# Kernel optimization log

Hardware: AMD Instinct MI355X
Metric: run time of the kernel (lower is better)

Reference implementation:

```python
import jax, jax.numpy as jnp
import numpy as np

B = 16384
FEAT_SIZES = [1000000, 1000000, 500000, 500000, 100000, 100000, 10000, 10000]
EMB_DIM = 50          # min(50, feat_size//2) for all chosen sizes
CONT_IN = 64
D = 8 * EMB_DIM + 64  # 464 = total_embedding_size + 64
H1, H2 = 256, 128     # expert/cross hidden sizes
E, T = 4, 3           # num_experts, num_tasks


def setup_inputs() -> dict:
    key = jax.random.key(0)
    ks = iter(jax.random.split(key, 64))
    s = 0.02
    inp = {}
    inp["discrete_features"] = jax.random.randint(next(ks), (B, 8), 0, 10000)
    inp["continuous_features"] = jax.random.normal(next(ks), (B, CONT_IN), jnp.float32)
    for i, fs in enumerate(FEAT_SIZES):
        inp[f"emb{i}"] = jax.random.normal(next(ks), (fs, EMB_DIM), jnp.float32) * s
    inp["cont_W"] = jax.random.normal(next(ks), (CONT_IN, 64), jnp.float32) * s
    inp["cont_b"] = jnp.zeros((64,), jnp.float32)
    inp["fm_W"] = jax.random.normal(next(ks), (D, 10), jnp.float32) * s
    inp["cW1"] = jax.random.normal(next(ks), (D, H1), jnp.float32) * s
    inp["cb1"] = jnp.zeros((H1,), jnp.float32)
    inp["cW2"] = jax.random.normal(next(ks), (H1, H2), jnp.float32) * s
    inp["cb2"] = jnp.zeros((H2,), jnp.float32)
    inp["coW"] = jax.random.normal(next(ks), (H2, D), jnp.float32) * s
    inp["cob"] = jnp.zeros((D,), jnp.float32)
    inp["expW1"] = jax.random.normal(next(ks), (E, D, H1), jnp.float32) * s
    inp["expb1"] = jnp.zeros((E, H1), jnp.float32)
    inp["expW2"] = jax.random.normal(next(ks), (E, H1, H2), jnp.float32) * s
    inp["expb2"] = jnp.zeros((E, H2), jnp.float32)
    inp["gate_W"] = jax.random.normal(next(ks), (T, D, E), jnp.float32) * s
    inp["gate_b"] = jnp.zeros((T, E), jnp.float32)
    inp["task_W"] = jax.random.normal(next(ks), (T, H2, 1), jnp.float32) * s
    inp["task_b"] = jnp.zeros((T, 1), jnp.float32)
    inp["log_vars"] = jnp.zeros((T,), jnp.float32)
    return inp


def reference(discrete_features, continuous_features,
              emb0, emb1, emb2, emb3, emb4, emb5, emb6, emb7,
              cont_W, cont_b, fm_W, cW1, cb1, cW2, cb2, coW, cob,
              expW1, expb1, expW2, expb2, gate_W, gate_b,
              task_W, task_b, log_vars):
    tables = [emb0, emb1, emb2, emb3, emb4, emb5, emb6, emb7]
    embs = [jnp.take(t, discrete_features[:, i], axis=0) for i, t in enumerate(tables)]
    cont = jax.nn.relu(continuous_features @ cont_W + cont_b)           # [B,64]
    x = jnp.concatenate(embs + [cont], axis=1)                          # [B,D]
    # FM part: x @ fm_embedding.weight -> [B,10], square-of-sum minus sum-of-square
    xe = x @ fm_W
    fm = 0.5 * (jnp.sum(xe, 1, keepdims=True) ** 2
                - jnp.sum(xe ** 2, 1, keepdims=True))                   # [B,1]
    # cross network
    c = jax.nn.relu(x @ cW1 + cb1)
    c = jax.nn.relu(c @ cW2 + cb2)
    co = c @ coW + cob                                                  # [B,D]
    h = x + co + fm                                                     # [B,D] (fm broadcast)
    # experts as batched GEMMs: [B,E,H2]
    e1 = jax.nn.relu(jnp.einsum('bd,edh->beh', h, expW1) + expb1)
    eo = jnp.einsum('beh,eho->beo', e1, expW2) + expb2
    # gates: [B,T,E] softmax over experts
    g = jax.nn.softmax(jnp.einsum('bd,tde->bte', h, gate_W) + gate_b, axis=-1)
    mixed = jnp.einsum('bte,beo->bto', g, eo)                           # [B,T,H2]
    out = jnp.einsum('bto,tok->btk', mixed, task_W) + task_b            # [B,T,1]
    return out[..., 0], log_vars                                        # ([B,3], [3])
```

## Files before the change

kernel.cpp:

```cpp
#include <hip/hip_runtime.h>
#include <stdint.h>

typedef _Float16 f16;
typedef __attribute__((ext_vector_type(8))) _Float16 f16x8;
typedef __attribute__((ext_vector_type(4))) float    f32x4;

constexpr int BROWS = 16384;
constexpr int NTASK = 3;

constexpr int OFF_CW1 = 0;
constexpr int OFF_CW2 = OFF_CW1 + 256 * 480;
constexpr int OFF_COW = OFF_CW2 + 128 * 256;
constexpr int OFF_EW1 = OFF_COW + 512 * 128;
constexpr int OFF_EW2 = OFF_EW1 + 1024 * 480;
constexpr int OFF_FMW = OFF_EW2 + 512 * 256;
constexpr int OFF_GW  = OFF_FMW + 16 * 480;
constexpr int OFF_CTW = OFF_GW  + 16 * 480;
constexpr int PACK_TOTAL = OFF_CTW + 64 * 64;

__global__ __launch_bounds__(256)
void pack_all(const float* __restrict__ cW1, const float* __restrict__ cW2,
              const float* __restrict__ coW, const float* __restrict__ expW1,
              const float* __restrict__ expW2, const float* __restrict__ fmW,
              const float* __restrict__ gateW, const float* __restrict__ contW,
              f16* __restrict__ wp)
{
    const int idx = blockIdx.x * 256 + threadIdx.x;
    if (idx >= PACK_TOTAL) return;
    float v = 0.f;
    if (idx < OFF_CW2) {
        const int l = idx - OFF_CW1, n = l / 480, k = l % 480;
        if (k < 464) v = cW1[k * 256 + n];
    } else if (idx < OFF_COW) {
        const int l = idx - OFF_CW2, n = l / 256, k = l % 256;
        v = cW2[k * 128 + n];
    } else if (idx < OFF_EW1) {
        const int l = idx - OFF_COW, n = l / 128, k = l % 128;
        if (n < 464) v = coW[k * 464 + n];
    } else if (idx < OFF_EW2) {
        const int l = idx - OFF_EW1, n = l / 480, k = l % 480;
        const int e = n >> 8, nn = n & 255;
        if (k < 464) v = expW1[(e * 464 + k) * 256 + nn];
    } else if (idx < OFF_FMW) {
        const int l = idx - OFF_EW2, n = l / 256, k = l % 256;
        const int e = n >> 7, nn = n & 127;
        v = expW2[(e * 256 + k) * 128 + nn];
    } else if (idx < OFF_GW) {
        const int l = idx - OFF_FMW, c = l / 480, k = l % 480;
        if (c < 10 && k < 464) v = fmW[k * 10 + c];
    } else if (idx < OFF_CTW) {
        const int l = idx - OFF_GW, c = l / 480, k = l % 480;
        if (c < 12 && k < 464) {
            const int tt = c >> 2, e = c & 3;
            v = gateW[(tt * 464 + k) * 4 + e];
        }
    } else {
        const int l = idx - OFF_CTW, n = l / 64, k = l % 64;
        v = contW[k * 64 + n];
    }
    wp[idx] = (f16)v;
}

template<int MF, int NF, int KS, int LDA>
__device__ __forceinline__ void wave_gemm(
    const f16* __restrict__ As, int arow0,
    const f16* __restrict__ Bg, int bcol0, int ldb,
    f32x4 (&acc)[MF][NF], int lane)
{
    const int g = lane >> 4, rr = lane & 15;
#pragma unroll
    for (int kb = 0; kb < KS; ++kb) {
        const int ko = kb * 32 + g * 8;
        f16x8 bf[NF];
#pragma unroll
        for (int j = 0; j < NF; ++j)
            bf[j] = *(const f16x8*)(Bg + (long)(bcol0 + j * 16 + rr) * ldb + ko);
#pragma unroll
        for (int i = 0; i < MF; ++i) {
            const f16x8 af = *(const f16x8*)(As + (arow0 + i * 16 + rr) * LDA + ko);
#pragma unroll
            for (int j = 0; j < NF; ++j)
                acc[i][j] = __builtin_amdgcn_mfma_f32_16x16x32_f16(
                    af, bf[j], acc[i][j], 0, 0, 0);
        }
    }
}

__global__ __launch_bounds__(256, 1)
void mmoe_fused(const int* __restrict__ disc, const float* __restrict__ cf,
                const float* __restrict__ e0p, const float* __restrict__ e1p,
                const float* __restrict__ e2p, const float* __restrict__ e3p,
                const float* __restrict__ e4p, const float* __restrict__ e5p,
                const float* __restrict__ e6p, const float* __restrict__ e7p,
                const float* __restrict__ contB, const float* __restrict__ cb1,
                const float* __restrict__ cb2, const float* __restrict__ cob,
                const float* __restrict__ expb1, const float* __restrict__ expb2,
                const float* __restrict__ gateB, const float* __restrict__ taskW,
                const float* __restrict__ taskB, const float* __restrict__ logv,
                const f16* __restrict__ wp, float* __restrict__ out)
{
    __shared__ f16   sh_x [64][488];
    __shared__ f16   sh_c1[64][264];
    __shared__ f16   sh_c2[64][136];
    __shared__ float sh_g [64][12];
    __shared__ float sh_part[4][64][3];
    __shared__ float sh_fm[64];
    __shared__ const float* stabs[8];

    const int t = threadIdx.x;
    const int lane = t & 63, wave = t >> 6;
    const int g = lane >> 4, rr = lane & 15;
    const long r0 = (long)blockIdx.x * 64;

    const f16* cW1p = wp + OFF_CW1;
    const f16* cW2p = wp + OFF_CW2;
    const f16* coWp = wp + OFF_COW;
    const f16* eW1p = wp + OFF_EW1;
    const f16* eW2p = wp + OFF_EW2;
    const f16* fmWp = wp + OFF_FMW;
    const f16* gWp  = wp + OFF_GW;
    const f16* ctWp = wp + OFF_CTW;

    if (t == 0) {
        stabs[0] = e0p; stabs[1] = e1p; stabs[2] = e2p; stabs[3] = e3p;
        stabs[4] = e4p; stabs[5] = e5p; stabs[6] = e6p; stabs[7] = e7p;
    }
    __syncthreads();

    f16* cfp = (f16*)&sh_c2[0][0];
    for (int i = t; i < 64 * 24; i += 256) sh_x[i / 24][464 + i % 24] = (f16)0.f;
    for (int p = t; p < 512; p += 256) {
        const int r = p >> 3, tab = p & 7;
        const long fi = disc[(r0 + r) * 8 + tab];
        const float* src = stabs[tab] + fi * 50;
        f16* dst = &sh_x[r][tab * 50];
#pragma unroll
        for (int q = 0; q < 25; ++q) {
            const float2 v = *(const float2*)(src + q * 2);
            dst[q * 2] = (f16)v.x; dst[q * 2 + 1] = (f16)v.y;
        }
    }
    for (int i = t; i < 64 * 16; i += 256) {
        const int r = i >> 4, q = i & 15;
        const float4 v = *(const float4*)(cf + (r0 + r) * 64 + q * 4);
        f16* dst = cfp + r * 72 + q * 4;
        dst[0] = (f16)v.x; dst[1] = (f16)v.y; dst[2] = (f16)v.z; dst[3] = (f16)v.w;
    }
    __syncthreads();

    {
        f32x4 acc[4][1] = {};
        wave_gemm<4, 1, 2, 72>(cfp, 0, ctWp, wave * 16, 64, acc, lane);
        const int col = wave * 16 + rr;
        const float bv = contB[col];
#pragma unroll
        for (int i = 0; i < 4; ++i)
#pragma unroll
            for (int rx = 0; rx < 4; ++rx)
                sh_x[i * 16 + g * 4 + rx][400 + col] =
                    (f16)fmaxf(acc[i][0][rx] + bv, 0.f);
    }
    __syncthreads();

    {
        f32x4 a[1][1] = {};
        wave_gemm<1, 1, 15, 488>(&sh_x[0][0], wave * 16, fmWp, 0, 480, a, lane);
#pragma unroll
        for (int rx = 0; rx < 4; ++rx) {
            const float v = a[0][0][rx];
            float s = v, ss = v * v;
#pragma unroll
            for (int off = 1; off < 16; off <<= 1) {
                s += __shfl_xor(s, off, 64); ss += __shfl_xor(ss, off, 64);
            }
            if (rr == 0) sh_fm[wave * 16 + g * 4 + rx] = 0.5f * (s * s - ss);
        }
    }
    {
        f32x4 acc[4][4] = {};
        wave_gemm<4, 4, 15, 488>(&sh_x[0][0], 0, cW1p, wave * 64, 480, acc, lane);
#pragma unroll
        for (int j = 0; j < 4; ++j) {
            const int col = wave * 64 + j * 16 + rr;
            const float bv = cb1[col];
#pragma unroll
            for (int i = 0; i < 4; ++i)
#pragma unroll
                for (int rx = 0; rx < 4; ++rx)
                    sh_c1[i * 16 + g * 4 + rx][col] =
                        (f16)fmaxf(acc[i][j][rx] + bv, 0.f);
        }
    }
    __syncthreads();

    {
        f32x4 acc[4][2] = {};
        wave_gemm<4, 2, 8, 264>(&sh_c1[0][0], 0, cW2p, wave * 32, 256, acc, lane);
#pragma unroll
        for (int j = 0; j < 2; ++j) {
            const int col = wave * 32 + j * 16 + rr;
            const float bv = cb2[col];
#pragma unroll
            for (int i = 0; i < 4; ++i)
#pragma unroll
                for (int rx = 0; rx < 4; ++rx)
                    sh_c2[i * 16 + g * 4 + rx][col] =
                        (f16)fmaxf(acc[i][j][rx] + bv, 0.f);
        }
    }
    __syncthreads();

    {
        f32x4 acc[4][8] = {};
        wave_gemm<4, 8, 4, 136>(&sh_c2[0][0], 0, coWp, wave * 128, 128, acc, lane);
#pragma unroll
        for (int j = 0; j < 8; ++j) {
            const int col = wave * 128 + j * 16 + rr;
            if (col < 464) {
                const float bv = cob[col];
#pragma unroll
                for (int i = 0; i < 4; ++i)
#pragma unroll
                    for (int rx = 0; rx < 4; ++rx) {
                        const int row = i * 16 + g * 4 + rx;
                        const float v = acc[i][j][rx] + bv +
                                        (float)sh_x[row][col] + sh_fm[row];
                        sh_x[row][col] = (f16)v;
                    }
            }
        }
    }
    __syncthreads();

    {
        f32x4 a[1][1] = {};
        wave_gemm<1, 1, 15, 488>(&sh_x[0][0], wave * 16, gWp, 0, 480, a, lane);
        const float gb = (rr < 12) ? gateB[rr] : 0.f;
#pragma unroll
        for (int rx = 0; rx < 4; ++rx) {
            const float v = a[0][0][rx] + gb;
            float m = fmaxf(v, __shfl_xor(v, 1, 64));
            m = fmaxf(m, __shfl_xor(m, 2, 64));
            const float p = __expf(v - m);
            float s = p + __shfl_xor(p, 1, 64);
            s += __shfl_xor(s, 2, 64);
            if (rr < 12) sh_g[wave * 16 + g * 4 + rx][rr] = p / s;
        }
    }
    __syncthreads();

    float tw[3][2];
#pragma unroll
    for (int tt = 0; tt < 3; ++tt) {
        tw[tt][0] = taskW[tt * 128 + wave * 32 + rr];
        tw[tt][1] = taskW[tt * 128 + wave * 32 + 16 + rr];
    }
    float oacc[4][4][3];
#pragma unroll
    for (int i = 0; i < 4; ++i)
#pragma unroll
        for (int rx = 0; rx < 4; ++rx)
#pragma unroll
            for (int tt = 0; tt < 3; ++tt) oacc[i][rx][tt] = 0.f;

#pragma unroll 1
    for (int e = 0; e < 4; ++e) {
        {
            f32x4 acc[4][4] = {};
            wave_gemm<4, 4, 15, 488>(&sh_x[0][0], 0, eW1p + e * (256 * 480),
                                     wave * 64, 480, acc, lane);
#pragma unroll
            for (int j = 0; j < 4; ++j) {
                const int col = wave * 64 + j * 16 + rr;
                const float bv = expb1[e * 256 + col];
#pragma unroll
                for (int i = 0; i < 4; ++i)
#pragma unroll
                    for (int rx = 0; rx < 4; ++rx)
                        sh_c1[i * 16 + g * 4 + rx][col] =
                            (f16)fmaxf(acc[i][j][rx] + bv, 0.f);
            }
        }
        __syncthreads();
        {
            f32x4 acc[4][2] = {};
            wave_gemm<4, 2, 8, 264>(&sh_c1[0][0], 0, eW2p + e * (128 * 256),
                                    wave * 32, 256, acc, lane);
            const float bv0 = expb2[e * 128 + wave * 32 + rr];
            const float bv1 = expb2[e * 128 + wave * 32 + 16 + rr];
#pragma unroll
            for (int i = 0; i < 4; ++i)
#pragma unroll
                for (int rx = 0; rx < 4; ++rx) {
                    const int row = i * 16 + g * 4 + rx;
                    const float v0 = acc[i][0][rx] + bv0;
                    const float v1 = acc[i][1][rx] + bv1;
#pragma unroll
                    for (int tt = 0; tt < 3; ++tt) {
                        float s = v0 * tw[tt][0] + v1 * tw[tt][1];
#pragma unroll
                        for (int off = 1; off < 16; off <<= 1)
                            s += __shfl_xor(s, off, 64);
                        oacc[i][rx][tt] += sh_g[row][tt * 4 + e] * s;
                    }
                }
        }
        __syncthreads();
    }

    if (rr == 0) {
#pragma unroll
        for (int i = 0; i < 4; ++i)
#pragma unroll
            for (int rx = 0; rx < 4; ++rx)
#pragma unroll
                for (int tt = 0; tt < 3; ++tt)
                    sh_part[wave][i * 16 + g * 4 + rx][tt] = oacc[i][rx][tt];
    }
    __syncthreads();
    for (int i = t; i < 64 * 3; i += 256) {
        const int row = i / 3, tt = i - row * 3;
        out[(r0 + row) * 3 + tt] = sh_part[0][row][tt] + sh_part[1][row][tt] +
                                   sh_part[2][row][tt] + sh_part[3][row][tt] +
                                   taskB[tt];
    }
    if (blockIdx.x == 0 && t < NTASK) out[(long)BROWS * 3 + t] = logv[t];
}

extern "C" void kernel_launch(void* const* d_in, const int* in_sizes, int n_in,
                              void* d_out, int out_size, void* d_ws, size_t ws_size,
                              hipStream_t stream)
{
    (void)in_sizes; (void)n_in; (void)out_size; (void)ws_size;

    const int*   disc  = (const int*)  d_in[0];
    const float* cf    = (const float*)d_in[1];
    const float* emb0  = (const float*)d_in[2];
    const float* emb1  = (const float*)d_in[3];
    const float* emb2  = (const float*)d_in[4];
    const float* emb3  = (const float*)d_in[5];
    const float* emb4  = (const float*)d_in[6];
    const float* emb5  = (const float*)d_in[7];
    const float* emb6  = (const float*)d_in[8];
    const float* emb7  = (const float*)d_in[9];
    const float* contW = (const float*)d_in[10];
    const float* contB = (const float*)d_in[11];
    const float* fmW   = (const float*)d_in[12];
    const float* cW1   = (const float*)d_in[13];
    const float* cb1   = (const float*)d_in[14];
    const float* cW2   = (const float*)d_in[15];
    const float* cb2   = (const float*)d_in[16];
    const float* coW   = (const float*)d_in[17];
    const float* cob   = (const float*)d_in[18];
    const float* expW1 = (const float*)d_in[19];
    const float* expb1 = (const float*)d_in[20];
    const float* expW2 = (const float*)d_in[21];
    const float* expb2 = (const float*)d_in[22];
    const float* gateW = (const float*)d_in[23];
    const float* gateB = (const float*)d_in[24];
    const float* taskW = (const float*)d_in[25];
    const float* taskB = (const float*)d_in[26];
    const float* logv  = (const float*)d_in[27];

    f16* wp = (f16*)d_ws;

    pack_all<<<(PACK_TOTAL + 255) / 256, 256, 0, stream>>>(
        cW1, cW2, coW, expW1, expW2, fmW, gateW, contW, wp);

    mmoe_fused<<<BROWS / 64, 256, 0, stream>>>(
        disc, cf, emb0, emb1, emb2, emb3, emb4, emb5, emb6, emb7,
        contB, cb1, cb2, cob, expb1, expb2, gateB, taskW, taskB, logv,
        wp, (float*)d_out);
}
```

Measured before the change: 100.7 us.

## Split fused MMoE kernel into pipelined per-layer GEMM kernels with packed tiles

Replaces the single fused per-64-row kernel with a chain of kernels: a gather/build kernel that also does the continuous and FM parts in fp32 scalar code, then separate 128x128-tile GEMM kernels for the cross layers, the residual h, experts layer 1 (with gates folded in as extra columns), and experts layer 2 with the task heads. Weights and activations are stored in an MFMA-fragment-packed layout and streamed into LDS with a triple-buffered global_load_lds pipeline. This is meant to raise weight reuse and occupancy over the old one-block-per-CU design. In exchange, intermediates make round trips through global memory and each extra launch adds overhead.

```diff
diff --git a/kernel.cpp b/kernel.cpp
--- a/kernel.cpp
+++ b/kernel.cpp
@@ -5,326 +5,403 @@
 typedef __attribute__((ext_vector_type(8))) _Float16 f16x8;
 typedef __attribute__((ext_vector_type(4))) float    f32x4;
 
-constexpr int BROWS = 16384;
-constexpr int NTASK = 3;
-
-constexpr int OFF_CW1 = 0;
-constexpr int OFF_CW2 = OFF_CW1 + 256 * 480;
-constexpr int OFF_COW = OFF_CW2 + 128 * 256;
-constexpr int OFF_EW1 = OFF_COW + 512 * 128;
-constexpr int OFF_EW2 = OFF_EW1 + 1024 * 480;
-constexpr int OFF_FMW = OFF_EW2 + 512 * 256;
-constexpr int OFF_GW  = OFF_FMW + 16 * 480;
-constexpr int OFF_CTW = OFF_GW  + 16 * 480;
-constexpr int PACK_TOTAL = OFF_CTW + 64 * 64;
-
-__global__ __launch_bounds__(256)
-void pack_all(const float* __restrict__ cW1, const float* __restrict__ cW2,
-              const float* __restrict__ coW, const float* __restrict__ expW1,
-              const float* __restrict__ expW2, const float* __restrict__ fmW,
-              const float* __restrict__ gateW, const float* __restrict__ contW,
-              f16* __restrict__ wp)
-{
-    const int idx = blockIdx.x * 256 + threadIdx.x;
-    if (idx >= PACK_TOTAL) return;
-    float v = 0.f;
-    if (idx < OFF_CW2) {
-        const int l = idx - OFF_CW1, n = l / 480, k = l % 480;
-        if (k < 464) v = cW1[k * 256 + n];
-    } else if (idx < OFF_COW) {
-        const int l = idx - OFF_CW2, n = l / 256, k = l % 256;
-        v = cW2[k * 128 + n];
-    } else if (idx < OFF_EW1) {
-        const int l = idx - OFF_COW, n = l / 128, k = l % 128;
-        if (n < 464) v = coW[k * 464 + n];
-    } else if (idx < OFF_EW2) {
-        const int l = idx - OFF_EW1, n = l / 480, k = l % 480;
-        const int e = n >> 8, nn = n & 255;
-        if (k < 464) v = expW1[(e * 464 + k) * 256 + nn];
-    } else if (idx < OFF_FMW) {
-        const int l = idx - OFF_EW2, n = l / 256, k = l % 256;
+constexpr int NB = 16384;
+
+constexpr int OFF_CW1  = 0;
+constexpr int OFF_CW2  = 122880;
+constexpr int OFF_COW  = 155648;
+constexpr int OFF_EW1G = 221184;
+constexpr int OFF_EW2  = 774144;
+constexpr int PACK_TOTAL = 905216;
+
+__device__ __forceinline__ void g2l16(const void* g, void* l) {
+    __builtin_amdgcn_global_load_lds(
+        (__attribute__((address_space(1))) void*)(void*)g,
+        (__attribute__((address_space(3))) void*)l, 16, 0, 0);
+}
+
+__global__ __launch_bounds__(256)
+void k_pack(const float* __restrict__ cW1, const float* __restrict__ cW2,
+            const float* __restrict__ coW, const float* __restrict__ expW1,
+            const float* __restrict__ expW2, const float* __restrict__ gateW,
+            f16* __restrict__ wp)
+{
+    const int lane = threadIdx.x & 63;
+    const int chunk = (blockIdx.x * 256 + threadIdx.x) >> 6;
+    if (chunk >= PACK_TOTAL / 512) return;
+    const int off = chunk * 512;
+    const int rr = lane & 15, gg = lane >> 4;
+    float v[8];
+    if (off < OFF_CW2) {
+        const int cl = off / 512, nt = cl / 15, kb = cl % 15;
+        const int n = nt * 16 + rr, k0 = kb * 32 + gg * 8;
+#pragma unroll
+        for (int q = 0; q < 8; ++q) { const int k = k0 + q; v[q] = (k < 464) ? cW1[k * 256 + n] : 0.f; }
+    } else if (off < OFF_COW) {
+        const int cl = (off - OFF_CW2) / 512, nt = cl / 8, kb = cl % 8;
+        const int n = nt * 16 + rr, k0 = kb * 32 + gg * 8;
+#pragma unroll
+        for (int q = 0; q < 8; ++q) v[q] = cW2[(k0 + q) * 128 + n];
+    } else if (off < OFF_EW1G) {
+        const int cl = (off - OFF_COW) / 512, nt = cl / 4, kb = cl % 4;
+        const int n = nt * 16 + rr, k0 = kb * 32 + gg * 8;
+#pragma unroll
+        for (int q = 0; q < 8; ++q) v[q] = (n < 464) ? coW[(k0 + q) * 464 + n] : 0.f;
+    } else if (off < OFF_EW2) {
+        const int cl = (off - OFF_EW1G) / 512, nt = cl / 15, kb = cl % 15;
+        const int n = nt * 16 + rr, k0 = kb * 32 + gg * 8;
+        if (n < 1024) {
+            const int e = n >> 8, nn = n & 255;
+#pragma unroll
+            for (int q = 0; q < 8; ++q) { const int k = k0 + q;
+                v[q] = (k < 464) ? expW1[((size_t)e * 464 + k) * 256 + nn] : 0.f; }
+        } else if (n < 1036) {
+            const int c = n - 1024;
+#pragma unroll
+            for (int q = 0; q < 8; ++q) { const int k = k0 + q;
+                v[q] = (k < 464) ? gateW[((size_t)(c >> 2) * 464 + k) * 4 + (c & 3)] : 0.f; }
+        } else {
+#pragma unroll
+            for (int q = 0; q < 8; ++q) v[q] = 0.f;
+        }
+    } else {
+        const int cl = (off - OFF_EW2) / 512, nt = cl / 8, kb = cl % 8;
+        const int n = nt * 16 + rr, k0 = kb * 32 + gg * 8;
         const int e = n >> 7, nn = n & 127;
-        v = expW2[(e * 256 + k) * 128 + nn];
-    } else if (idx < OFF_GW) {
-        const int l = idx - OFF_FMW, c = l / 480, k = l % 480;
-        if (c < 10 && k < 464) v = fmW[k * 10 + c];
-    } else if (idx < OFF_CTW) {
-        const int l = idx - OFF_GW, c = l / 480, k = l % 480;
-        if (c < 12 && k < 464) {
-            const int tt = c >> 2, e = c & 3;
-            v = gateW[(tt * 464 + k) * 4 + e];
-        }
-    } else {
-        const int l = idx - OFF_CTW, n = l / 64, k = l % 64;
-        v = contW[k * 64 + n];
-    }
-    wp[idx] = (f16)v;
-}
-
-template<int MF, int NF, int KS, int LDA>
-__device__ __forceinline__ void wave_gemm(
-    const f16* __restrict__ As, int arow0,
-    const f16* __restrict__ Bg, int bcol0, int ldb,
-    f32x4 (&acc)[MF][NF], int lane)
-{
-    const int g = lane >> 4, rr = lane & 15;
-#pragma unroll
-    for (int kb = 0; kb < KS; ++kb) {
-        const int ko = kb * 32 + g * 8;
-        f16x8 bf[NF];
-#pragma unroll
-        for (int j = 0; j < NF; ++j)
-            bf[j] = *(const f16x8*)(Bg + (long)(bcol0 + j * 16 + rr) * ldb + ko);
-#pragma unroll
-        for (int i = 0; i < MF; ++i) {
-            const f16x8 af = *(const f16x8*)(As + (arow0 + i * 16 + rr) * LDA + ko);
-#pragma unroll
-            for (int j = 0; j < NF; ++j)
-                acc[i][j] = __builtin_amdgcn_mfma_f32_16x16x32_f16(
-                    af, bf[j], acc[i][j], 0, 0, 0);
-        }
-    }
-}
-
-__global__ __launch_bounds__(256, 1)
-void mmoe_fused(const int* __restrict__ disc, const float* __restrict__ cf,
-                const float* __restrict__ e0p, const float* __restrict__ e1p,
-                const float* __restrict__ e2p, const float* __restrict__ e3p,
-                const float* __restrict__ e4p, const float* __restrict__ e5p,
-                const float* __restrict__ e6p, const float* __restrict__ e7p,
-                const float* __restrict__ contB, const float* __restrict__ cb1,
-                const float* __restrict__ cb2, const float* __restrict__ cob,
-                const float* __restrict__ expb1, const float* __restrict__ expb2,
-                const float* __restrict__ gateB, const float* __restrict__ taskW,
-                const float* __restrict__ taskB, const float* __restrict__ logv,
-                const f16* __restrict__ wp, float* __restrict__ out)
-{
-    __shared__ f16   sh_x [64][488];
-    __shared__ f16   sh_c1[64][264];
-    __shared__ f16   sh_c2[64][136];
-    __shared__ float sh_g [64][12];
-    __shared__ float sh_part[4][64][3];
-    __shared__ float sh_fm[64];
+#pragma unroll
+        for (int q = 0; q < 8; ++q) v[q] = expW2[((size_t)e * 256 + q + k0) * 128 + nn];
+    }
+    f16x8 o;
+#pragma unroll
+    for (int q = 0; q < 8; ++q) o[q] = (f16)v[q];
+    *(f16x8*)(wp + (size_t)off + lane * 8) = o;
+}
+
+__global__ __launch_bounds__(256)
+void k_build(const int* __restrict__ disc, const float* __restrict__ cf,
+             const float* __restrict__ e0p, const float* __restrict__ e1p,
+             const float* __restrict__ e2p, const float* __restrict__ e3p,
+             const float* __restrict__ e4p, const float* __restrict__ e5p,
+             const float* __restrict__ e6p, const float* __restrict__ e7p,
+             const float* __restrict__ contW, const float* __restrict__ contB,
+             const float* __restrict__ fmW,
+             f16* __restrict__ xpk, float* __restrict__ fm)
+{
+    __shared__ f16   xs[64][480];
+    __shared__ float cfs[64][68];
+    __shared__ float ctw[64][64];
+    __shared__ float fmw[4640];
+    __shared__ float xes[64][10];
     __shared__ const float* stabs[8];
 
     const int t = threadIdx.x;
-    const int lane = t & 63, wave = t >> 6;
-    const int g = lane >> 4, rr = lane & 15;
     const long r0 = (long)blockIdx.x * 64;
-
-    const f16* cW1p = wp + OFF_CW1;
-    const f16* cW2p = wp + OFF_CW2;
-    const f16* coWp = wp + OFF_COW;
-    const f16* eW1p = wp + OFF_EW1;
-    const f16* eW2p = wp + OFF_EW2;
-    const f16* fmWp = wp + OFF_FMW;
-    const f16* gWp  = wp + OFF_GW;
-    const f16* ctWp = wp + OFF_CTW;
-
     if (t == 0) {
         stabs[0] = e0p; stabs[1] = e1p; stabs[2] = e2p; stabs[3] = e3p;
         stabs[4] = e4p; stabs[5] = e5p; stabs[6] = e6p; stabs[7] = e7p;
     }
     __syncthreads();
 
-    f16* cfp = (f16*)&sh_c2[0][0];
-    for (int i = t; i < 64 * 24; i += 256) sh_x[i / 24][464 + i % 24] = (f16)0.f;
+    for (int i = t; i < 64 * 16; i += 256) xs[i >> 4][464 + (i & 15)] = (f16)0.f;
+    for (int i = t; i < 64 * 16; i += 256) {
+        const int r = i >> 4, q = i & 15;
+        const float4 v = *(const float4*)(cf + (r0 + r) * 64 + q * 4);
+        cfs[r][q * 4] = v.x; cfs[r][q * 4 + 1] = v.y; cfs[r][q * 4 + 2] = v.z; cfs[r][q * 4 + 3] = v.w;
+    }
+    for (int i = t; i < 1024; i += 256) {
+        const int k = i >> 4, c4 = (i & 15) * 4;
+        *(float4*)&ctw[k][c4] = *(const float4*)(contW + k * 64 + c4);
+    }
+    for (int i = t; i < 4640; i += 256) fmw[i] = fmW[i];
     for (int p = t; p < 512; p += 256) {
         const int r = p >> 3, tab = p & 7;
         const long fi = disc[(r0 + r) * 8 + tab];
         const float* src = stabs[tab] + fi * 50;
-        f16* dst = &sh_x[r][tab * 50];
+        f16* dst = &xs[r][tab * 50];
 #pragma unroll
         for (int q = 0; q < 25; ++q) {
             const float2 v = *(const float2*)(src + q * 2);
             dst[q * 2] = (f16)v.x; dst[q * 2 + 1] = (f16)v.y;
         }
     }
-    for (int i = t; i < 64 * 16; i += 256) {
-        const int r = i >> 4, q = i & 15;
-        const float4 v = *(const float4*)(cf + (r0 + r) * 64 + q * 4);
-        f16* dst = cfp + r * 72 + q * 4;
-        dst[0] = (f16)v.x; dst[1] = (f16)v.y; dst[2] = (f16)v.z; dst[3] = (f16)v.w;
-    }
-    __syncthreads();
-
-    {
-        f32x4 acc[4][1] = {};
-        wave_gemm<4, 1, 2, 72>(cfp, 0, ctWp, wave * 16, 64, acc, lane);
-        const int col = wave * 16 + rr;
-        const float bv = contB[col];
+    __syncthreads();
+    for (int i = t; i < 4096; i += 256) {
+        const int r = i >> 6, c = i & 63;
+        float a = contB[c];
+#pragma unroll 8
+        for (int k = 0; k < 64; ++k) a = fmaf(cfs[r][k], ctw[k][c], a);
+        xs[r][400 + c] = (f16)fmaxf(a, 0.f);
+    }
+    __syncthreads();
+    for (int i = t; i < 640; i += 256) {
+        const int r = i / 10, jj = i - (i / 10) * 10;
+        float a = 0.f;
+        for (int d = 0; d < 464; ++d) a = fmaf((float)xs[r][d], fmw[d * 10 + jj], a);
+        xes[r][jj] = a;
+    }
+    __syncthreads();
+    if (t < 64) {
+        float s = 0.f, ss = 0.f;
+#pragma unroll
+        for (int j = 0; j < 10; ++j) { const float v = xes[t][j]; s += v; ss += v * v; }
+        fm[r0 + t] = 0.5f * (s * s - ss);
+    }
+    for (int si = t; si < 3840; si += 256) {
+        const int rt = si / 960, rem = si - rt * 960;
+        const int kb = rem >> 6, slot = rem & 63;
+        const int gg = slot >> 4, rr2 = slot & 15;
+        *(f16x8*)(xpk + ((size_t)(blockIdx.x * 4 + rt) * 15 + kb) * 512 + slot * 8)
+            = *(const f16x8*)&xs[rt * 16 + rr2][kb * 32 + gg * 8];
+    }
+}
+
+template<int KB>
+__device__ __forceinline__ void gemm_pipe(
+    const f16* __restrict__ Apk, size_t ach0,
+    const f16* __restrict__ Bpk, int nt0,
+    f16* lA, f16* lB, f32x4 (&acc)[4][4],
+    int wave, int lane, int wm, int wn, int g, int rr)
+{
+    auto issue = [&](int kb) {
+        const int buf = kb % 3;
+#pragma unroll
+        for (int h2 = 0; h2 < 2; ++h2) {
+            const int rt = 2 * wave + h2;
+            g2l16(Apk + (ach0 + (size_t)rt * KB + kb) * 512 + lane * 8,
+                  lA + (size_t)buf * 4096 + rt * 512);
+            g2l16(Bpk + ((size_t)(nt0 + rt) * KB + kb) * 512 + lane * 8,
+                  lB + (size_t)buf * 4096 + rt * 512);
+        }
+    };
+    issue(0); issue(1);
+#pragma unroll
+    for (int kb = 0; kb < KB; ++kb) {
+        if (kb < KB - 1) asm volatile("s_waitcnt vmcnt(4)" ::: "memory");
+        else             asm volatile("s_waitcnt vmcnt(0)" ::: "memory");
+        __builtin_amdgcn_s_barrier();
+        __builtin_amdgcn_sched_barrier(0);
+        if (kb + 2 < KB) issue(kb + 2);
+        const f16* A_ = lA + (size_t)(kb % 3) * 4096;
+        const f16* B_ = lB + (size_t)(kb % 3) * 4096;
+        f16x8 bf[4];
+#pragma unroll
+        for (int j = 0; j < 4; ++j)
+            bf[j] = *(const f16x8*)(B_ + ((wn * 4 + j) * 64 + g * 16 + rr) * 8);
+#pragma unroll
+        for (int i = 0; i < 4; ++i) {
+            const f16x8 af = *(const f16x8*)(A_ + ((wm * 4 + i) * 64 + g * 16 + rr) * 8);
+#pragma unroll
+            for (int j = 0; j < 4; ++j)
+                acc[i][j] = __builtin_amdgcn_mfma_f32_16x16x32_f16(af, bf[j], acc[i][j], 0, 0, 0);
+        }
+    }
+    __syncthreads();
+}
+
+#define GEMM_PRE() \
+    __shared__ __align__(16) f16 lbuf[24576]; \
+    const int t = threadIdx.x, lane = t & 63, wave = t >> 6; \
+    const int wm = wave >> 1, wn = wave & 1, g = lane >> 4, rr = lane & 15; \
+    const int by = blockIdx.y, ct = blockIdx.x; (void)ct; (void)t; \
+    f32x4 acc[4][4] = {};
+
+__global__ __launch_bounds__(256)
+void k_c1(const f16* __restrict__ wp, const f16* __restrict__ xpk,
+          const float* __restrict__ cb1, f16* __restrict__ c1pk)
+{
+    GEMM_PRE();
+    gemm_pipe<15>(xpk, (size_t)by * 120, wp + OFF_CW1, ct * 8,
+                  lbuf, lbuf + 12288, acc, wave, lane, wm, wn, g, rr);
+    const int rowb = by * 128 + wm * 64;
+#pragma unroll
+    for (int j = 0; j < 4; ++j) {
+        const int col = ct * 128 + wn * 64 + j * 16 + rr;
+        const float bv = cb1[col];
+        const int kbo = col >> 5, go = (col >> 3) & 3, qo = col & 7;
 #pragma unroll
         for (int i = 0; i < 4; ++i)
 #pragma unroll
-            for (int rx = 0; rx < 4; ++rx)
-                sh_x[i * 16 + g * 4 + rx][400 + col] =
-                    (f16)fmaxf(acc[i][0][rx] + bv, 0.f);
-    }
-    __syncthreads();
-
-    {
-        f32x4 a[1][1] = {};
-        wave_gemm<1, 1, 15, 488>(&sh_x[0][0], wave * 16, fmWp, 0, 480, a, lane);
-#pragma unroll
-        for (int rx = 0; rx < 4; ++rx) {
-            const float v = a[0][0][rx];
-            float s = v, ss = v * v;
+            for (int rg = 0; rg < 4; ++rg) {
+                const int row = rowb + i * 16 + g * 4 + rg;
+                c1pk[(((size_t)(row >> 4) * 8 + kbo) * 64 + go * 16 + (row & 15)) * 8 + qo]
+                    = (f16)fmaxf(acc[i][j][rg] + bv, 0.f);
+            }
+    }
+}
+
+__global__ __launch_bounds__(256)
+void k_c2(const f16* __restrict__ wp, const f16* __restrict__ c1pk,
+          const float* __restrict__ cb2, f16* __restrict__ c2pk)
+{
+    GEMM_PRE();
+    gemm_pipe<8>(c1pk, (size_t)by * 64, wp + OFF_CW2, 0,
+                 lbuf, lbuf + 12288, acc, wave, lane, wm, wn, g, rr);
+    const int rowb = by * 128 + wm * 64;
+#pragma unroll
+    for (int j = 0; j < 4; ++j) {
+        const int col = wn * 64 + j * 16 + rr;
+        const float bv = cb2[col];
+        const int kbo = col >> 5, go = (col >> 3) & 3, qo = col & 7;
+#pragma unroll
+        for (int i = 0; i < 4; ++i)
+#pragma unroll
+            for (int rg = 0; rg < 4; ++rg) {
+                const int row = rowb + i * 16 + g * 4 + rg;
+                c2pk[(((size_t)(row >> 4) * 4 + kbo) * 64 + go * 16 + (row & 15)) * 8 + qo]
+                    = (f16)fmaxf(acc[i][j][rg] + bv, 0.f);
+            }
+    }
+}
+
+__global__ __launch_bounds__(256)
+void k_h(const f16* __restrict__ wp, const f16* __restrict__ c2pk,
+         const float* __restrict__ cob, const float* __restrict__ fm,
+         f16* __restrict__ xpk)
+{
+    GEMM_PRE();
+    gemm_pipe<4>(c2pk, (size_t)by * 32, wp + OFF_COW, ct * 8,
+                 lbuf, lbuf + 12288, acc, wave, lane, wm, wn, g, rr);
+    const int ct4 = ct * 4;
+    for (int c = wave; c < 32; c += 4) {
+        const int rt_l = c >> 2, kbl = c & 3;
+        if (ct4 + kbl < 15)
+            g2l16(xpk + ((size_t)(by * 8 + rt_l) * 15 + ct4 + kbl) * 512 + lane * 8,
+                  lbuf + (size_t)c * 512);
+    }
+    asm volatile("s_waitcnt vmcnt(0)" ::: "memory");
+    __syncthreads();
+    const int rowb = by * 128 + wm * 64;
+#pragma unroll
+    for (int j = 0; j < 4; ++j) {
+        const int col = ct * 128 + wn * 64 + j * 16 + rr;
+        if (col < 464) {
+            const float bv = cob[col];
+            const int kbl = (col >> 5) & 3, go = (col >> 3) & 3, qo = col & 7;
+#pragma unroll
+            for (int i = 0; i < 4; ++i)
+#pragma unroll
+                for (int rg = 0; rg < 4; ++rg) {
+                    const int row = rowb + i * 16 + g * 4 + rg;
+                    const int cc = (wm * 4 + i) * 4 + kbl;
+                    const float xv = (float)lbuf[((size_t)cc * 64 + go * 16 + (g * 4 + rg)) * 8 + qo];
+                    const float hv = acc[i][j][rg] + bv + xv + fm[row];
+                    xpk[(((size_t)(row >> 4) * 15 + (col >> 5)) * 64 + go * 16 + (row & 15)) * 8 + qo]
+                        = (f16)hv;
+                }
+        }
+    }
+}
+
+__global__ __launch_bounds__(256)
+void k_e1(const f16* __restrict__ wp, const f16* __restrict__ xpk,
+          const float* __restrict__ expb1, const float* __restrict__ gateB,
+          f16* __restrict__ e1pk, float* __restrict__ gates)
+{
+    GEMM_PRE();
+    gemm_pipe<15>(xpk, (size_t)by * 120, wp + OFF_EW1G, ct * 8,
+                  lbuf, lbuf + 12288, acc, wave, lane, wm, wn, g, rr);
+    const int rowb = by * 128 + wm * 64;
+    if (ct < 8) {
+#pragma unroll
+        for (int j = 0; j < 4; ++j) {
+            const int col = ct * 128 + wn * 64 + j * 16 + rr;
+            const int e = col >> 8, cl = col & 255;
+            const float bv = expb1[col];
+            const int kbo = cl >> 5, go = (cl >> 3) & 3, qo = cl & 7;
+            f16* dst = e1pk + (size_t)e * NB * 256;
+#pragma unroll
+            for (int i = 0; i < 4; ++i)
+#pragma unroll
+                for (int rg = 0; rg < 4; ++rg) {
+                    const int row = rowb + i * 16 + g * 4 + rg;
+                    dst[(((size_t)(row >> 4) * 8 + kbo) * 64 + go * 16 + (row & 15)) * 8 + qo]
+                        = (f16)fmaxf(acc[i][j][rg] + bv, 0.f);
+                }
+        }
+    } else if (wn == 0) {
+        const float gb = (rr < 12) ? gateB[rr] : 0.f;
+#pragma unroll
+        for (int i = 0; i < 4; ++i)
+#pragma unroll
+            for (int rg = 0; rg < 4; ++rg) {
+                const float v = acc[i][0][rg] + gb;
+                float m = fmaxf(v, __shfl_xor(v, 1, 64));
+                m = fmaxf(m, __shfl_xor(m, 2, 64));
+                const float p = __expf(v - m);
+                float s = p + __shfl_xor(p, 1, 64);
+                s += __shfl_xor(s, 2, 64);
+                if (rr < 12) {
+                    const long row = rowb + i * 16 + g * 4 + rg;
+                    gates[row * 12 + rr] = p / s;
+                }
+            }
+    }
+}
+
+__global__ __launch_bounds__(256)
+void k_e2(const f16* __restrict__ wp, const f16* __restrict__ e1pk,
+          const float* __restrict__ expb2, const float* __restrict__ taskW,
+          const float* __restrict__ gates, float* __restrict__ part)
+{
+    GEMM_PRE();
+    __shared__ float sh_s[2][2][64][3];
+    const int z = blockIdx.z;
+    gemm_pipe<8>(e1pk + (size_t)z * NB * 256, (size_t)by * 64, wp + OFF_EW2, z * 8,
+                 lbuf, lbuf + 12288, acc, wave, lane, wm, wn, g, rr);
+    float tws[3][4], bj[4];
+#pragma unroll
+    for (int j = 0; j < 4; ++j) {
+        const int col = wn * 64 + j * 16 + rr;
+        bj[j] = expb2[z * 128 + col];
+#pragma unroll
+        for (int tt = 0; tt < 3; ++tt) tws[tt][j] = taskW[tt * 128 + col];
+    }
+#pragma unroll
+    for (int i = 0; i < 4; ++i)
+#pragma unroll
+        for (int rg = 0; rg < 4; ++rg) {
+            float p0 = 0.f, p1 = 0.f, p2 = 0.f;
+#pragma unroll
+            for (int j = 0; j < 4; ++j) {
+                const float v = acc[i][j][rg] + bj[j];
+                p0 = fmaf(v, tws[0][j], p0);
+                p1 = fmaf(v, tws[1][j], p1);
+                p2 = fmaf(v, tws[2][j], p2);
+            }
 #pragma unroll
             for (int off = 1; off < 16; off <<= 1) {
-                s += __shfl_xor(s, off, 64); ss += __shfl_xor(ss, off, 64);
-            }
-            if (rr == 0) sh_fm[wave * 16 + g * 4 + rx] = 0.5f * (s * s - ss);
-        }
-    }
-    {
-        f32x4 acc[4][4] = {};
-        wave_gemm<4, 4, 15, 488>(&sh_x[0][0], 0, cW1p, wave * 64, 480, acc, lane);
-#pragma unroll
-        for (int j = 0; j < 4; ++j) {
-            const int col = wave * 64 + j * 16 + rr;
-            const float bv = cb1[col];
-#pragma unroll
-            for (int i = 0; i < 4; ++i)
-#pragma unroll
-                for (int rx = 0; rx < 4; ++rx)
-                    sh_c1[i * 16 + g * 4 + rx][col] =
-                        (f16)fmaxf(acc[i][j][rx] + bv, 0.f);
-        }
-    }
-    __syncthreads();
-
-    {
-        f32x4 acc[4][2] = {};
-        wave_gemm<4, 2, 8, 264>(&sh_c1[0][0], 0, cW2p, wave * 32, 256, acc, lane);
-#pragma unroll
-        for (int j = 0; j < 2; ++j) {
-            const int col = wave * 32 + j * 16 + rr;
-            const float bv = cb2[col];
-#pragma unroll
-            for (int i = 0; i < 4; ++i)
-#pragma unroll
-                for (int rx = 0; rx < 4; ++rx)
-                    sh_c2[i * 16 + g * 4 + rx][col] =
-                        (f16)fmaxf(acc[i][j][rx] + bv, 0.f);
-        }
-    }
-    __syncthreads();
-
-    {
-        f32x4 acc[4][8] = {};
-        wave_gemm<4, 8, 4, 136>(&sh_c2[0][0], 0, coWp, wave * 128, 128, acc, lane);
-#pragma unroll
-        for (int j = 0; j < 8; ++j) {
-            const int col = wave * 128 + j * 16 + rr;
-            if (col < 464) {
-                const float bv = cob[col];
-#pragma unroll
-                for (int i = 0; i < 4; ++i)
-#pragma unroll
-                    for (int rx = 0; rx < 4; ++rx) {
-                        const int row = i * 16 + g * 4 + rx;
-                        const float v = acc[i][j][rx] + bv +
-                                        (float)sh_x[row][col] + sh_fm[row];
-                        sh_x[row][col] = (f16)v;
-                    }
-            }
-        }
-    }
-    __syncthreads();
-
-    {
-        f32x4 a[1][1] = {};
-        wave_gemm<1, 1, 15, 488>(&sh_x[0][0], wave * 16, gWp, 0, 480, a, lane);
-        const float gb = (rr < 12) ? gateB[rr] : 0.f;
-#pragma unroll
-        for (int rx = 0; rx < 4; ++rx) {
-            const float v = a[0][0][rx] + gb;
-            float m = fmaxf(v, __shfl_xor(v, 1, 64));
-            m = fmaxf(m, __shfl_xor(m, 2, 64));
-            const float p = __expf(v - m);
-            float s = p + __shfl_xor(p, 1, 64);
-            s += __shfl_xor(s, 2, 64);
-            if (rr < 12) sh_g[wave * 16 + g * 4 + rx][rr] = p / s;
-        }
-    }
-    __syncthreads();
-
-    float tw[3][2];
-#pragma unroll
-    for (int tt = 0; tt < 3; ++tt) {
-        tw[tt][0] = taskW[tt * 128 + wave * 32 + rr];
-        tw[tt][1] = taskW[tt * 128 + wave * 32 + 16 + rr];
-    }
-    float oacc[4][4][3];
-#pragma unroll
-    for (int i = 0; i < 4; ++i)
-#pragma unroll
-        for (int rx = 0; rx < 4; ++rx)
-#pragma unroll
-            for (int tt = 0; tt < 3; ++tt) oacc[i][rx][tt] = 0.f;
-
-#pragma unroll 1
-    for (int e = 0; e < 4; ++e) {
-        {
-            f32x4 acc[4][4] = {};
-            wave_gemm<4, 4, 15, 488>(&sh_x[0][0], 0, eW1p + e * (256 * 480),
-                                     wave * 64, 480, acc, lane);
-#pragma unroll
-            for (int j = 0; j < 4; ++j) {
-                const int col = wave * 64 + j * 16 + rr;
-                const float bv = expb1[e * 256 + col];
-#pragma unroll
-                for (int i = 0; i < 4; ++i)
-#pragma unroll
-                    for (int rx = 0; rx < 4; ++rx)
-                        sh_c1[i * 16 + g * 4 + rx][col] =
-                            (f16)fmaxf(acc[i][j][rx] + bv, 0.f);
-            }
-        }
-        __syncthreads();
-        {
-            f32x4 acc[4][2] = {};
-            wave_gemm<4, 2, 8, 264>(&sh_c1[0][0], 0, eW2p + e * (128 * 256),
-                                    wave * 32, 256, acc, lane);
-            const float bv0 = expb2[e * 128 + wave * 32 + rr];
-            const float bv1 = expb2[e * 128 + wave * 32 + 16 + rr];
-#pragma unroll
-            for (int i = 0; i < 4; ++i)
-#pragma unroll
-                for (int rx = 0; rx < 4; ++rx) {
-                    const int row = i * 16 + g * 4 + rx;
-                    const float v0 = acc[i][0][rx] + bv0;
-                    const float v1 = acc[i][1][rx] + bv1;
-#pragma unroll
-                    for (int tt = 0; tt < 3; ++tt) {
-                        float s = v0 * tw[tt][0] + v1 * tw[tt][1];
-#pragma unroll
-                        for (int off = 1; off < 16; off <<= 1)
-                            s += __shfl_xor(s, off, 64);
-                        oacc[i][rx][tt] += sh_g[row][tt * 4 + e] * s;
-                    }
-                }
-        }
-        __syncthreads();
-    }
-
-    if (rr == 0) {
-#pragma unroll
-        for (int i = 0; i < 4; ++i)
-#pragma unroll
-            for (int rx = 0; rx < 4; ++rx)
-#pragma unroll
-                for (int tt = 0; tt < 3; ++tt)
-                    sh_part[wave][i * 16 + g * 4 + rx][tt] = oacc[i][rx][tt];
-    }
-    __syncthreads();
-    for (int i = t; i < 64 * 3; i += 256) {
-        const int row = i / 3, tt = i - row * 3;
-        out[(r0 + row) * 3 + tt] = sh_part[0][row][tt] + sh_part[1][row][tt] +
-                                   sh_part[2][row][tt] + sh_part[3][row][tt] +
-                                   taskB[tt];
-    }
-    if (blockIdx.x == 0 && t < NTASK) out[(long)BROWS * 3 + t] = logv[t];
+                p0 += __shfl_xor(p0, off, 64);
+                p1 += __shfl_xor(p1, off, 64);
+                p2 += __shfl_xor(p2, off, 64);
+            }
+            if (rr == 0) {
+                const int rl = i * 16 + g * 4 + rg;
+                sh_s[wm][wn][rl][0] = p0; sh_s[wm][wn][rl][1] = p1; sh_s[wm][wn][rl][2] = p2;
+            }
+        }
+    __syncthreads();
+    for (int idx = t; idx < 128 * 3; idx += 256) {
+        const int rl = idx / 3, tt = idx - rl * 3;
+        const int wmm = rl >> 6, r2 = rl & 63;
+        const float s = sh_s[wmm][0][r2][tt] + sh_s[wmm][1][r2][tt];
+        const long row = (long)by * 128 + rl;
+        part[((size_t)z * NB + row) * 3 + tt] = gates[row * 12 + tt * 4 + z] * s;
+    }
+}
+
+__global__ __launch_bounds__(256)
+void k_final(const float* __restrict__ part, const float* __restrict__ taskB,
+             const float* __restrict__ logv, float* __restrict__ out)
+{
+    const int idx = blockIdx.x * 256 + threadIdx.x;
+    if (idx < NB * 3) {
+        const int row = idx / 3, tt = idx - row * 3;
+        out[idx] = part[(size_t)row * 3 + tt] +
+                   part[(size_t)NB * 3 + row * 3 + tt] +
+                   part[(size_t)NB * 6 + row * 3 + tt] +
+                   part[(size_t)NB * 9 + row * 3 + tt] + taskB[tt];
+    }
+    if (idx < 3) out[(size_t)NB * 3 + idx] = logv[idx];
 }
 
 extern "C" void kernel_launch(void* const* d_in, const int* in_sizes, int n_in,
@@ -362,13 +439,24 @@
     const float* taskB = (const float*)d_in[26];
     const float* logv  = (const float*)d_in[27];
 
-    f16* wp = (f16*)d_ws;
-
-    pack_all<<<(PACK_TOTAL + 255) / 256, 256, 0, stream>>>(
-        cW1, cW2, coW, expW1, expW2, fmW, gateW, contW, wp);
-
-    mmoe_fused<<<BROWS / 64, 256, 0, stream>>>(
+    char* w = (char*)d_ws;
+    f16* wp     = (f16*)w;   w += (size_t)PACK_TOTAL * 2;
+    f16* xpk    = (f16*)w;   w += (size_t)NB * 480 * 2;
+    f16* c1pk   = (f16*)w;   w += (size_t)NB * 256 * 2;
+    f16* c2pk   = (f16*)w;   w += (size_t)NB * 128 * 2;
+    f16* e1pk   = (f16*)w;   w += (size_t)4 * NB * 256 * 2;
+    float* fm   = (float*)w; w += (size_t)NB * 4;
+    float* gates= (float*)w; w += (size_t)NB * 12 * 4;
+    float* part = (float*)w; w += (size_t)4 * NB * 3 * 4;
+
+    k_pack<<<442, 256, 0, stream>>>(cW1, cW2, coW, expW1, expW2, gateW, wp);
+    k_build<<<NB / 64, 256, 0, stream>>>(
         disc, cf, emb0, emb1, emb2, emb3, emb4, emb5, emb6, emb7,
-        contB, cb1, cb2, cob, expb1, expb2, gateB, taskW, taskB, logv,
-        wp, (float*)d_out);
-}
+        contW, contB, fmW, xpk, fm);
+    k_c1<<<dim3(2, 128), 256, 0, stream>>>(wp, xpk, cb1, c1pk);
+    k_c2<<<dim3(1, 128), 256, 0, stream>>>(wp, c1pk, cb2, c2pk);
+    k_h <<<dim3(4, 128), 256, 0, stream>>>(wp, c2pk, cob, fm, xpk);
+    k_e1<<<dim3(9, 128), 256, 0, stream>>>(wp, xpk, expb1, gateB, e1pk, gates);
+    k_e2<<<dim3(1, 128, 4), 256, 0, stream>>>(wp, e1pk, expb2, taskW, gates, part);
+    k_final<<<192, 256, 0, stream>>>(part, taskB, logv, (float*)d_out);
+}
```

Result: slower. 138.7 us (+37.7%).
